# Optimization experiments

Hardware: AMD Instinct MI355X
Metric: run time of the kernel (lower is better)

Reference implementation:

```python
import jax, jax.numpy as jnp
import numpy as np

N = 50000
NEG_SLOPE = 0.2  # PyG GATConv default negative_slope


def gat_conv(x, src, dst, W, a_src, a_dst, bias, concat):
    """One PyG-style GATConv (eval mode, self-loops already in src/dst).
    x: [N, F_in], W: [F_in, H*C], a_src/a_dst: [H, C], bias: [H*C] or [C].
    """
    H, C = a_src.shape
    xl = (x @ W).reshape(N, H, C)                      # [N, H, C]
    alpha_src = jnp.sum(xl * a_src, axis=-1)           # [N, H]
    alpha_dst = jnp.sum(xl * a_dst, axis=-1)           # [N, H]
    e = jax.nn.leaky_relu(alpha_src[src] + alpha_dst[dst], NEG_SLOPE)  # [E, H]
    # edge-softmax over incoming edges of each destination node
    m = jax.ops.segment_max(e, dst, num_segments=N)    # [N, H]
    e = jnp.exp(e - m[dst])
    s = jax.ops.segment_sum(e, dst, num_segments=N)    # [N, H]
    alpha = e / s[dst]                                 # [E, H]
    msg = xl[src] * alpha[:, :, None]                  # [E, H, C]
    out = jax.ops.segment_sum(msg, dst, num_segments=N)  # [N, H, C]
    out = out.reshape(N, H * C) if concat else out.mean(axis=1)
    return out + bias


def setup_inputs() -> dict:
    key = jax.random.key(0)
    ks = jax.random.split(key, 10)
    in_ch, hid, out_ch, heads = 128, 64, 64, 4
    E = 800000
    x = jax.random.normal(ks[0], (N, in_ch), dtype=jnp.float32)
    edge_index = jax.random.randint(ks[1], (2, E), 0, N, dtype=jnp.int64)
    s1 = 1.0 / np.sqrt(in_ch)
    s2 = 1.0 / np.sqrt(hid * heads)
    return {
        "x": x,
        "edge_index": edge_index,
        "W1": jax.random.normal(ks[2], (in_ch, heads * hid), jnp.float32) * s1,
        "att_src1": jax.random.normal(ks[3], (heads, hid), jnp.float32) * s1,
        "att_dst1": jax.random.normal(ks[4], (heads, hid), jnp.float32) * s1,
        "b1": jnp.zeros((heads * hid,), jnp.float32),
        "W2": jax.random.normal(ks[5], (heads * hid, out_ch), jnp.float32) * s2,
        "att_src2": jax.random.normal(ks[6], (1, out_ch), jnp.float32) * s2,
        "att_dst2": jax.random.normal(ks[7], (1, out_ch), jnp.float32) * s2,
        "b2": jnp.zeros((out_ch,), jnp.float32),
    }


def reference(x, edge_index, W1, att_src1, att_dst1, b1, W2, att_src2, att_dst2, b2):
    # PyG GATConv adds self-loops by default
    loops = jnp.arange(N, dtype=edge_index.dtype)
    src = jnp.concatenate([edge_index[0], loops])
    dst = jnp.concatenate([edge_index[1], loops])
    h = gat_conv(x, src, dst, W1, att_src1, att_dst1, b1, concat=True)
    h = jax.nn.elu(h)  # dropout is identity in eval mode
    out = gat_conv(h, src, dst, W2, att_src2, att_dst2, b2, concat=False)
    return out
```

## Files before the change

### kernel.cpp

```cpp
#include <hip/hip_runtime.h>
#include <math.h>


typedef unsigned short u16;
typedef short s8v __attribute__((ext_vector_type(8)));
typedef float f32x4 __attribute__((ext_vector_type(4)));

#define LOG2E 1.4426950408889634f

__device__ __forceinline__ float bflo(unsigned int u) {
  return __builtin_bit_cast(float, u << 16);
}
__device__ __forceinline__ float bfhi(unsigned int u) {
  return __builtin_bit_cast(float, u & 0xffff0000u);
}
__device__ __forceinline__ u16 f2bf(float f) {
  unsigned int u = __builtin_bit_cast(unsigned int, f);
  return (u16)((u + 0x7fff + ((u >> 16) & 1)) >> 16);
}


__global__ void count_edges_kernel(const int* __restrict__ ei, int E, int Nn,
                                   int* __restrict__ deg) {
  int e = blockIdx.x * blockDim.x + threadIdx.x;
  if (e >= E + Nn) return;
  int dst = (e < E) ? ei[E + e] : (e - E);
  atomicAdd(&deg[dst], 1);
}

__global__ void scan_partials_kernel(const int* __restrict__ deg,
                                     int* __restrict__ partials, int Ntot) {
  __shared__ int red[256];
  int t = threadIdx.x;
  int base = blockIdx.x * 1024 + t * 4;
  int s = 0;
  if (base + 3 < Ntot) {
    int4 v = *(const int4*)(deg + base);
    s = v.x + v.y + v.z + v.w;
  } else {
    for (int i = 0; i < 4; ++i)
      if (base + i < Ntot) s += deg[base + i];
  }
  red[t] = s;
  __syncthreads();
  for (int off = 128; off > 0; off >>= 1) {
    if (t < off) red[t] += red[t + off];
    __syncthreads();
  }
  if (t == 0) partials[blockIdx.x] = red[0];
}

__global__ void scan_final_kernel(const int* __restrict__ deg,
                                  const int* __restrict__ partials,
                                  int* __restrict__ rowptr,
                                  int* __restrict__ cursor, int Ntot, int NB) {
  __shared__ int sums[256];
  int t = threadIdx.x;
  int bid = blockIdx.x;
  int base = bid * 1024 + t * 4;
  int4 v = make_int4(0, 0, 0, 0);
  if (base + 3 < Ntot) {
    v = *(const int4*)(deg + base);
  } else {
    if (base + 0 < Ntot) v.x = deg[base + 0];
    if (base + 1 < Ntot) v.y = deg[base + 1];
    if (base + 2 < Ntot) v.z = deg[base + 2];
    if (base + 3 < Ntot) v.w = deg[base + 3];
  }
  sums[t] = v.x + v.y + v.z + v.w;
  __syncthreads();
  for (int off = 1; off < 256; off <<= 1) {
    int u = (t >= off) ? sums[t - off] : 0;
    __syncthreads();
    sums[t] += u;
    __syncthreads();
  }
  int boff = 0;
  for (int j = 0; j < bid; ++j) boff += partials[j];
  int excl = boff + ((t == 0) ? 0 : sums[t - 1]);
  int4 r;
  r.x = excl;
  r.y = r.x + v.x;
  r.z = r.y + v.y;
  r.w = r.z + v.z;
  if (base + 3 < Ntot) {
    *(int4*)(rowptr + base) = r;
    *(int4*)(cursor + base) = r;
  } else {
    if (base + 0 < Ntot) { rowptr[base + 0] = r.x; cursor[base + 0] = r.x; }
    if (base + 1 < Ntot) { rowptr[base + 1] = r.y; cursor[base + 1] = r.y; }
    if (base + 2 < Ntot) { rowptr[base + 2] = r.z; cursor[base + 2] = r.z; }
    if (base + 3 < Ntot) { rowptr[base + 3] = r.w; cursor[base + 3] = r.w; }
  }
}

__global__ void scatter_edges_kernel(const int* __restrict__ ei, int E, int Nn,
                                     int* __restrict__ cursor, int* __restrict__ col) {
  int e = blockIdx.x * blockDim.x + threadIdx.x;
  if (e >= E + Nn) return;
  int src, dst;
  if (e < E) { src = ei[e]; dst = ei[E + e]; }
  else       { src = dst = e - E; }
  int pos = atomicAdd(&cursor[dst], 1);
  col[pos] = src;
}


__global__ void cast_prep_kernel(const float* __restrict__ x, u16* __restrict__ xb,
                                 int nx4,
                                 const float* __restrict__ W1, u16* __restrict__ W1T,
                                 int K1, int N1,
                                 const float* __restrict__ W2, u16* __restrict__ W2T,
                                 int K2, int N2) {
  int i = blockIdx.x * blockDim.x + threadIdx.x;
  if (i < nx4) {
    float4 v = *(const float4*)(x + (size_t)i * 4);
    ushort4 o = make_ushort4(f2bf(v.x), f2bf(v.y), f2bf(v.z), f2bf(v.w));
    *(ushort4*)(xb + (size_t)i * 4) = o;
    return;
  }
  int e = i - nx4;
  int tot1 = K1 * N1;
  if (e < tot1) {
    int k = e / N1, n = e % N1;
    W1T[n * K1 + k] = f2bf(W1[e]);
    return;
  }
  e -= tot1;
  if (e < K2 * N2) {
    int k = e / N2, n = e % N2;
    W2T[n * K2 + k] = f2bf(W2[e]);
  }
}


template <int BN>
__global__ __launch_bounds__(256) void gemm_mfma_kernel(
    const u16* __restrict__ A, const u16* __restrict__ Bt,
    u16* __restrict__ C, int M, int K, int NC) {
  constexpr int BM = 128, BK = 32, PK = 40;
  constexpr int NJ = BN / 32;
  __shared__ short As[BM][PK];
  __shared__ short Bs[BN][PK];

  int tid = threadIdx.x;
  int lane = tid & 63, w = tid >> 6;
  int wm = (w >> 1) * 64, wn = (w & 1) * (BN / 2);
  int bm0 = blockIdx.x * BM, bn0 = blockIdx.y * BN;
  int fr = lane & 15, fk = (lane >> 4) * 8;

  f32x4 acc[4][NJ] = {};

  for (int k0 = 0; k0 < K; k0 += BK) {
#pragma unroll
    for (int p = 0; p < BM * BK / 2048; ++p) {
      int idx = p * 2048 + tid * 8;
      int r = idx / BK, c = idx % BK;
      *(s8v*)&As[r][c] = *(const s8v*)(A + (size_t)(bm0 + r) * K + k0 + c);
    }
#pragma unroll
    for (int p = 0; p < BN * BK / 2048; ++p) {
      int idx = p * 2048 + tid * 8;
      int r = idx / BK, c = idx % BK;
      *(s8v*)&Bs[r][c] = *(const s8v*)(Bt + (size_t)(bn0 + r) * K + k0 + c);
    }
    __syncthreads();

    s8v af[4], bf[NJ];
#pragma unroll
    for (int i = 0; i < 4; ++i)
      af[i] = *(const s8v*)&As[wm + i * 16 + fr][fk];
#pragma unroll
    for (int j = 0; j < NJ; ++j)
      bf[j] = *(const s8v*)&Bs[wn + j * 16 + fr][fk];
#pragma unroll
    for (int i = 0; i < 4; ++i)
#pragma unroll
      for (int j = 0; j < NJ; ++j)
        acc[i][j] = __builtin_amdgcn_mfma_f32_16x16x32_bf16(af[i], bf[j], acc[i][j], 0, 0, 0);
    __syncthreads();
  }

#pragma unroll
  for (int i = 0; i < 4; ++i)
#pragma unroll
    for (int j = 0; j < NJ; ++j)
#pragma unroll
      for (int r = 0; r < 4; ++r) {
        int row = bm0 + wm + i * 16 + (lane >> 4) * 4 + r;
        if (row < M)
          C[(size_t)row * NC + bn0 + wn + j * 16 + fr] = f2bf(acc[i][j][r]);
      }
}


__global__ void alpha_kernel(const u16* __restrict__ xlb,
                             const float* __restrict__ a_src,
                             const float* __restrict__ a_dst,
                             float* __restrict__ asrc, float* __restrict__ adst,
                             int NH, int H, int C) {
  int idx = blockIdx.x * blockDim.x + threadIdx.x;
  if (idx >= NH) return;
  int h = idx % H;
  const u16* row = xlb + (size_t)idx * C;
  float ssum = 0.f, dsum = 0.f;
  for (int c = 0; c < C; c += 8) {
    uint4 v = *(const uint4*)(row + c);
    float f[8] = {bflo(v.x), bfhi(v.x), bflo(v.y), bfhi(v.y),
                  bflo(v.z), bfhi(v.z), bflo(v.w), bfhi(v.w)};
#pragma unroll
    for (int j = 0; j < 8; ++j) {
      ssum = fmaf(f[j], a_src[h * C + c + j], ssum);
      dsum = fmaf(f[j], a_dst[h * C + c + j], dsum);
    }
  }
  asrc[idx] = ssum * LOG2E;
  adst[idx] = dsum * LOG2E;
}


__global__ void agg_multi_kernel(const u16* __restrict__ xlb,
                                 const float* __restrict__ asrc,
                                 const float* __restrict__ adst,
                                 const int* __restrict__ rowptr,
                                 const int* __restrict__ col,
                                 const float* __restrict__ bias,
                                 u16* __restrict__ hb, int Nn) {
  int n = blockIdx.x * 8 + (threadIdx.x >> 5);
  if (n >= Nn) return;
  int lane = threadIdx.x & 31;
  int h = lane >> 3;
  float adn = adst[n * 4 + h];
  int beg = rowptr[n], end = rowptr[n + 1];

  float s = 0.f;
  float acc[8] = {};

  float as0 = 0.f, as1 = 0.f, as2 = 0.f, as3 = 0.f;
  uint4 v0 = {}, v1 = {}, v2 = {}, v3 = {};
  {
    int sc = col[beg];
    as0 = asrc[sc * 4 + h];
    v0 = *(const uint4*)(xlb + (size_t)sc * 256 + lane * 8);
    if (beg + 1 < end) {
      int c1 = col[beg + 1];
      as1 = asrc[c1 * 4 + h];
      v1 = *(const uint4*)(xlb + (size_t)c1 * 256 + lane * 8);
    }
    if (beg + 2 < end) {
      int c2 = col[beg + 2];
      as2 = asrc[c2 * 4 + h];
      v2 = *(const uint4*)(xlb + (size_t)c2 * 256 + lane * 8);
    }
    if (beg + 3 < end) {
      int c3 = col[beg + 3];
      as3 = asrc[c3 * 4 + h];
      v3 = *(const uint4*)(xlb + (size_t)c3 * 256 + lane * 8);
    }
  }

  for (int i = beg; i < end; ++i) {
    float e = as0 + adn;
    e = fmaxf(e, 0.2f * e);
    uint4 vc = v0;
    as0 = as1; v0 = v1;
    as1 = as2; v1 = v2;
    as2 = as3; v2 = v3;
    if (i + 4 < end) {
      int sc = col[i + 4];
      as3 = asrc[sc * 4 + h];
      v3 = *(const uint4*)(xlb + (size_t)sc * 256 + lane * 8);
    }
    float w = __builtin_amdgcn_exp2f(e);
    s += w;
    acc[0] = fmaf(w, bflo(vc.x), acc[0]);
    acc[1] = fmaf(w, bfhi(vc.x), acc[1]);
    acc[2] = fmaf(w, bflo(vc.y), acc[2]);
    acc[3] = fmaf(w, bfhi(vc.y), acc[3]);
    acc[4] = fmaf(w, bflo(vc.z), acc[4]);
    acc[5] = fmaf(w, bfhi(vc.z), acc[5]);
    acc[6] = fmaf(w, bflo(vc.w), acc[6]);
    acc[7] = fmaf(w, bfhi(vc.w), acc[7]);
  }
  float inv_s = 1.f / s;

  float4 b0 = *(const float4*)(bias + lane * 8);
  float4 b1f = *(const float4*)(bias + lane * 8 + 4);
  float bb[8] = {b0.x, b0.y, b0.z, b0.w, b1f.x, b1f.y, b1f.z, b1f.w};
  u16 ov[8];
#pragma unroll
  for (int j = 0; j < 8; ++j) {
    float o = fmaf(acc[j], inv_s, bb[j]);
    o = (o > 0.f) ? o : __expf(o) - 1.f;
    ov[j] = f2bf(o);
  }
  *(uint4*)(hb + (size_t)n * 256 + lane * 8) = *(uint4*)ov;
}


__global__ void agg_single_kernel(const u16* __restrict__ xlb,
                                  const float* __restrict__ asrc,
                                  const float* __restrict__ adst,
                                  const int* __restrict__ rowptr,
                                  const int* __restrict__ col,
                                  const float* __restrict__ bias,
                                  float* __restrict__ out, int Nn) {
  int n = blockIdx.x * 32 + (threadIdx.x >> 3);
  if (n >= Nn) return;
  int lane = threadIdx.x & 7;
  float adn = adst[n];
  int beg = rowptr[n], end = rowptr[n + 1];

  float s = 0.f;
  float acc[8] = {};

  float as0 = 0.f, as1 = 0.f, as2 = 0.f;
  uint4 v0 = {}, v1 = {}, v2 = {};
  {
    int sc = col[beg];
    as0 = asrc[sc];
    v0 = *(const uint4*)(xlb + (size_t)sc * 64 + lane * 8);
    if (beg + 1 < end) {
      int c1 = col[beg + 1];
      as1 = asrc[c1];
      v1 = *(const uint4*)(xlb + (size_t)c1 * 64 + lane * 8);
    }
    if (beg + 2 < end) {
      int c2 = col[beg + 2];
      as2 = asrc[c2];
      v2 = *(const uint4*)(xlb + (size_t)c2 * 64 + lane * 8);
    }
  }

  for (int i = beg; i < end; ++i) {
    float e = as0 + adn;
    e = fmaxf(e, 0.2f * e);
    uint4 vc = v0;
    as0 = as1; v0 = v1;
    as1 = as2; v1 = v2;
    if (i + 3 < end) {
      int sc = col[i + 3];
      as2 = asrc[sc];
      v2 = *(const uint4*)(xlb + (size_t)sc * 64 + lane * 8);
    }
    float w = __builtin_amdgcn_exp2f(e);
    s += w;
    acc[0] = fmaf(w, bflo(vc.x), acc[0]);
    acc[1] = fmaf(w, bfhi(vc.x), acc[1]);
    acc[2] = fmaf(w, bflo(vc.y), acc[2]);
    acc[3] = fmaf(w, bfhi(vc.y), acc[3]);
    acc[4] = fmaf(w, bflo(vc.z), acc[4]);
    acc[5] = fmaf(w, bfhi(vc.z), acc[5]);
    acc[6] = fmaf(w, bflo(vc.w), acc[6]);
    acc[7] = fmaf(w, bfhi(vc.w), acc[7]);
  }
  float inv_s = 1.f / s;

  const float* bp = bias + lane * 8;
  float4 o0, o1;
  o0.x = fmaf(acc[0], inv_s, bp[0]);
  o0.y = fmaf(acc[1], inv_s, bp[1]);
  o0.z = fmaf(acc[2], inv_s, bp[2]);
  o0.w = fmaf(acc[3], inv_s, bp[3]);
  o1.x = fmaf(acc[4], inv_s, bp[4]);
  o1.y = fmaf(acc[5], inv_s, bp[5]);
  o1.z = fmaf(acc[6], inv_s, bp[6]);
  o1.w = fmaf(acc[7], inv_s, bp[7]);
  *(float4*)(out + (size_t)n * 64 + lane * 8) = o0;
  *(float4*)(out + (size_t)n * 64 + lane * 8 + 4) = o1;
}


extern "C" void kernel_launch(void* const* d_in, const int* in_sizes, int n_in,
                              void* d_out, int out_size, void* d_ws, size_t ws_size,
                              hipStream_t stream) {
  const float* x   = (const float*)d_in[0];
  const int*   ei  = (const int*)d_in[1];
  const float* W1  = (const float*)d_in[2];
  const float* as1 = (const float*)d_in[3];
  const float* ad1 = (const float*)d_in[4];
  const float* b1  = (const float*)d_in[5];
  const float* W2  = (const float*)d_in[6];
  const float* as2 = (const float*)d_in[7];
  const float* ad2 = (const float*)d_in[8];
  const float* b2  = (const float*)d_in[9];
  float* out = (float*)d_out;

  const int Nn = in_sizes[0] / 128;
  const int E  = in_sizes[1] / 2;
  const int Et = E + Nn;
  const int Ntot = Nn + 1;
  const int NB = (Ntot + 1023) / 1024;
  const int MB = (Nn + 127) / 128;
  const int Mpad = MB * 128;

  char* base = (char*)d_ws;
  size_t off = 0;
  auto alloc = [&](size_t bytes) -> void* {
    void* p = base + off;
    off = (off + bytes + 255) & ~(size_t)255;
    return p;
  };
  u16*   xb       = (u16*)alloc((size_t)Mpad * 128 * 2);
  u16*   w1t      = (u16*)alloc((size_t)256 * 128 * 2);
  u16*   w2t      = (u16*)alloc((size_t)64 * 256 * 2);
  u16*   xlb1     = (u16*)alloc((size_t)Mpad * 256 * 2);
  u16*   hb       = (u16*)alloc((size_t)Mpad * 256 * 2);
  float* asrc1    = (float*)alloc((size_t)Nn * 4 * 4);
  float* adst1    = (float*)alloc((size_t)Nn * 4 * 4);
  float* asrc2    = (float*)alloc((size_t)Nn * 4);
  float* adst2    = (float*)alloc((size_t)Nn * 4);
  int*   deg      = (int*)alloc((size_t)(Ntot + 8) * 4);
  int*   rowptr   = (int*)alloc((size_t)(Ntot + 8) * 4);
  int*   cursor   = (int*)alloc((size_t)(Ntot + 8) * 4);
  int*   partials = (int*)alloc(256 * 4);
  int*   col      = (int*)alloc((size_t)Et * 4);
  u16*   xlb2     = xlb1;

  hipMemsetAsync(deg, 0, (size_t)Ntot * 4, stream);
  count_edges_kernel<<<(Et + 255) / 256, 256, 0, stream>>>(ei, E, Nn, deg);
  scan_partials_kernel<<<NB, 256, 0, stream>>>(deg, partials, Ntot);
  scan_final_kernel<<<NB, 256, 0, stream>>>(deg, partials, rowptr, cursor, Ntot, NB);
  scatter_edges_kernel<<<(Et + 255) / 256, 256, 0, stream>>>(ei, E, Nn, cursor, col);
  {
    int nx4 = Nn * 128 / 4;
    int tot = nx4 + 128 * 256 + 256 * 64;
    cast_prep_kernel<<<(tot + 255) / 256, 256, 0, stream>>>(
        x, xb, nx4, W1, w1t, 128, 256, W2, w2t, 256, 64);
  }

  {
    dim3 grid(MB, 2);
    gemm_mfma_kernel<128><<<grid, 256, 0, stream>>>(xb, w1t, xlb1, Nn, 128, 256);
  }
  alpha_kernel<<<(Nn * 4 + 255) / 256, 256, 0, stream>>>(xlb1, as1, ad1, asrc1, adst1, Nn * 4, 4, 64);
  agg_multi_kernel<<<(Nn + 7) / 8, 256, 0, stream>>>(xlb1, asrc1, adst1, rowptr, col, b1, hb, Nn);

  {
    dim3 grid(MB, 1);
    gemm_mfma_kernel<64><<<grid, 256, 0, stream>>>(hb, w2t, xlb2, Nn, 256, 64);
  }
  alpha_kernel<<<(Nn + 255) / 256, 256, 0, stream>>>(xlb2, as2, ad2, asrc2, adst2, Nn, 1, 64);
  agg_single_kernel<<<(Nn + 31) / 32, 256, 0, stream>>>(xlb2, asrc2, adst2, rowptr, col, b2, out, Nn);
}
```

Measured before the change: 260.0 us.

## Fuse x cast into GEMM1 and attention-logit dot products into both GEMM epilogues

Drops the separate fp32-to-bf16 cast pass over x by converting rows while loading them into GEMM1's shared memory, with the whole K=128 held in LDS at once. Computes the per-head source and destination attention logits in the GEMM epilogues from the fp32 accumulators using lane shuffles, which removes both alpha kernels and their re-read of xl. Weight transposition moves into the edge-count kernel. This cuts launches and global traffic, but GEMM1 now uses more shared memory per block (lower occupancy), and the logits come from fp32 accumulators instead of bf16-rounded values.

Result: faster. 254.0 us (-2.3%).

```diff
diff --git a/kernel.cpp b/kernel.cpp
--- a/kernel.cpp
+++ b/kernel.cpp
@@ -20,12 +20,28 @@
 }
 
 
-__global__ void count_edges_kernel(const int* __restrict__ ei, int E, int Nn,
-                                   int* __restrict__ deg) {
-  int e = blockIdx.x * blockDim.x + threadIdx.x;
-  if (e >= E + Nn) return;
-  int dst = (e < E) ? ei[E + e] : (e - E);
-  atomicAdd(&deg[dst], 1);
+__global__ void prep_count_kernel(const int* __restrict__ ei, int E, int Nn,
+                                  int* __restrict__ deg,
+                                  const float* __restrict__ W1, u16* __restrict__ W1T,
+                                  const float* __restrict__ W2, u16* __restrict__ W2T) {
+  int i = blockIdx.x * blockDim.x + threadIdx.x;
+  int Et = E + Nn;
+  if (i < Et) {
+    int dst = (i < E) ? ei[E + i] : (i - E);
+    atomicAdd(&deg[dst], 1);
+    return;
+  }
+  int e = i - Et;
+  if (e < 128 * 256) {
+    int k = e >> 8, n = e & 255;
+    W1T[n * 128 + k] = f2bf(W1[e]);
+    return;
+  }
+  e -= 128 * 256;
+  if (e < 256 * 64) {
+    int k = e >> 6, n = e & 63;
+    W2T[n * 256 + k] = f2bf(W2[e]);
+  }
 }
 
 __global__ void scan_partials_kernel(const int* __restrict__ deg,
@@ -106,116 +122,209 @@
 }
 
 
-__global__ void cast_prep_kernel(const float* __restrict__ x, u16* __restrict__ xb,
-                                 int nx4,
-                                 const float* __restrict__ W1, u16* __restrict__ W1T,
-                                 int K1, int N1,
-                                 const float* __restrict__ W2, u16* __restrict__ W2T,
-                                 int K2, int N2) {
-  int i = blockIdx.x * blockDim.x + threadIdx.x;
-  if (i < nx4) {
-    float4 v = *(const float4*)(x + (size_t)i * 4);
+__global__ __launch_bounds__(256) void gemm1_fused_kernel(
+    const float* __restrict__ x,
+    const u16* __restrict__ w1t,
+    const float* __restrict__ a_src,
+    const float* __restrict__ a_dst,
+    u16* __restrict__ C,
+    float* __restrict__ asrc, float* __restrict__ adst,
+    int M) {
+  constexpr int PK = 136;
+  __shared__ short As[128][PK];
+  __shared__ short Bs[128][PK];
+  int tid = threadIdx.x;
+  int lane = tid & 63, w = tid >> 6;
+  int q = lane >> 4, fr = lane & 15;
+  int wm = (w >> 1) * 64, wn = (w & 1) * 64;
+  int bm0 = blockIdx.x * 128;
+  int fk = q * 8;
+
+#pragma unroll
+  for (int p = 0; p < 16; ++p) {
+    int idx = p * 1024 + tid * 4;
+    int r = idx >> 7, c = idx & 127;
+    float4 v = make_float4(0.f, 0.f, 0.f, 0.f);
+    if (bm0 + r < M) v = *(const float4*)(x + (size_t)(bm0 + r) * 128 + c);
     ushort4 o = make_ushort4(f2bf(v.x), f2bf(v.y), f2bf(v.z), f2bf(v.w));
-    *(ushort4*)(xb + (size_t)i * 4) = o;
-    return;
-  }
-  int e = i - nx4;
-  int tot1 = K1 * N1;
-  if (e < tot1) {
-    int k = e / N1, n = e % N1;
-    W1T[n * K1 + k] = f2bf(W1[e]);
-    return;
-  }
-  e -= tot1;
-  if (e < K2 * N2) {
-    int k = e / N2, n = e % N2;
-    W2T[n * K2 + k] = f2bf(W2[e]);
-  }
-}
-
-
-template <int BN>
-__global__ __launch_bounds__(256) void gemm_mfma_kernel(
-    const u16* __restrict__ A, const u16* __restrict__ Bt,
-    u16* __restrict__ C, int M, int K, int NC) {
-  constexpr int BM = 128, BK = 32, PK = 40;
-  constexpr int NJ = BN / 32;
+    *(ushort4*)&As[r][c] = o;
+  }
+#pragma unroll
+  for (int p = 0; p < 8; ++p) {
+    int idx = p * 2048 + tid * 8;
+    int r = idx >> 7, c = idx & 127;
+    *(s8v*)&Bs[r][c] = *(const s8v*)(w1t + (size_t)r * 128 + c);
+  }
+  __syncthreads();
+
+  for (int nh = 0; nh < 2; ++nh) {
+    if (nh == 1) {
+      __syncthreads();
+#pragma unroll
+      for (int p = 0; p < 8; ++p) {
+        int idx = p * 2048 + tid * 8;
+        int r = idx >> 7, c = idx & 127;
+        *(s8v*)&Bs[r][c] = *(const s8v*)(w1t + (size_t)(128 + r) * 128 + c);
+      }
+      __syncthreads();
+    }
+    f32x4 acc[4][4] = {};
+#pragma unroll
+    for (int ks = 0; ks < 4; ++ks) {
+      s8v af[4], bf[4];
+#pragma unroll
+      for (int i = 0; i < 4; ++i)
+        af[i] = *(const s8v*)&As[wm + i * 16 + fr][ks * 32 + fk];
+#pragma unroll
+      for (int j = 0; j < 4; ++j)
+        bf[j] = *(const s8v*)&Bs[wn + j * 16 + fr][ks * 32 + fk];
+#pragma unroll
+      for (int i = 0; i < 4; ++i)
+#pragma unroll
+        for (int j = 0; j < 4; ++j)
+          acc[i][j] = __builtin_amdgcn_mfma_f32_16x16x32_bf16(af[i], bf[j], acc[i][j], 0, 0, 0);
+    }
+
+    int h = nh * 2 + (wn >> 6);
+    float asv[4], adv[4];
+#pragma unroll
+    for (int j = 0; j < 4; ++j) {
+      asv[j] = a_src[h * 64 + j * 16 + fr];
+      adv[j] = a_dst[h * 64 + j * 16 + fr];
+    }
+#pragma unroll
+    for (int i = 0; i < 4; ++i) {
+#pragma unroll
+      for (int r = 0; r < 4; ++r) {
+        int row = bm0 + wm + i * 16 + q * 4 + r;
+        float ps = 0.f, pd = 0.f;
+#pragma unroll
+        for (int j = 0; j < 4; ++j) {
+          ps = fmaf(acc[i][j][r], asv[j], ps);
+          pd = fmaf(acc[i][j][r], adv[j], pd);
+        }
+#pragma unroll
+        for (int mmask = 1; mmask < 16; mmask <<= 1) {
+          ps += __shfl_xor(ps, mmask, 64);
+          pd += __shfl_xor(pd, mmask, 64);
+        }
+        if (fr == 0 && row < M) {
+          asrc[row * 4 + h] = ps * LOG2E;
+          adst[row * 4 + h] = pd * LOG2E;
+        }
+      }
+    }
+#pragma unroll
+    for (int i = 0; i < 4; ++i)
+#pragma unroll
+      for (int j = 0; j < 4; ++j)
+#pragma unroll
+        for (int r = 0; r < 4; ++r) {
+          int row = bm0 + wm + i * 16 + q * 4 + r;
+          if (row < M)
+            C[(size_t)row * 256 + nh * 128 + wn + j * 16 + fr] = f2bf(acc[i][j][r]);
+        }
+  }
+}
+
+
+__global__ __launch_bounds__(256) void gemm2_fused_kernel(
+    const u16* __restrict__ A,
+    const u16* __restrict__ Bt,
+    const float* __restrict__ a_src,
+    const float* __restrict__ a_dst,
+    u16* __restrict__ C,
+    float* __restrict__ asrc, float* __restrict__ adst,
+    int M) {
+  constexpr int BM = 128, BN = 64, BK = 32, PK = 40;
   __shared__ short As[BM][PK];
   __shared__ short Bs[BN][PK];
-
+  __shared__ float alds[BM][4];
   int tid = threadIdx.x;
   int lane = tid & 63, w = tid >> 6;
-  int wm = (w >> 1) * 64, wn = (w & 1) * (BN / 2);
-  int bm0 = blockIdx.x * BM, bn0 = blockIdx.y * BN;
-  int fr = lane & 15, fk = (lane >> 4) * 8;
-
-  f32x4 acc[4][NJ] = {};
-
-  for (int k0 = 0; k0 < K; k0 += BK) {
-#pragma unroll
-    for (int p = 0; p < BM * BK / 2048; ++p) {
+  int q = lane >> 4, fr = lane & 15;
+  int wm = (w >> 1) * 64, wn = (w & 1) * 32;
+  int bm0 = blockIdx.x * BM;
+  int fk = q * 8;
+
+  f32x4 acc[4][2] = {};
+
+  for (int k0 = 0; k0 < 256; k0 += BK) {
+#pragma unroll
+    for (int p = 0; p < 2; ++p) {
       int idx = p * 2048 + tid * 8;
       int r = idx / BK, c = idx % BK;
-      *(s8v*)&As[r][c] = *(const s8v*)(A + (size_t)(bm0 + r) * K + k0 + c);
-    }
-#pragma unroll
-    for (int p = 0; p < BN * BK / 2048; ++p) {
-      int idx = p * 2048 + tid * 8;
+      *(s8v*)&As[r][c] = *(const s8v*)(A + (size_t)(bm0 + r) * 256 + k0 + c);
+    }
+    {
+      int idx = tid * 8;
       int r = idx / BK, c = idx % BK;
-      *(s8v*)&Bs[r][c] = *(const s8v*)(Bt + (size_t)(bn0 + r) * K + k0 + c);
+      if (r < BN)
+        *(s8v*)&Bs[r][c] = *(const s8v*)(Bt + (size_t)r * 256 + k0 + c);
     }
     __syncthreads();
 
-    s8v af[4], bf[NJ];
+    s8v af[4], bf[2];
 #pragma unroll
     for (int i = 0; i < 4; ++i)
       af[i] = *(const s8v*)&As[wm + i * 16 + fr][fk];
 #pragma unroll
-    for (int j = 0; j < NJ; ++j)
+    for (int j = 0; j < 2; ++j)
       bf[j] = *(const s8v*)&Bs[wn + j * 16 + fr][fk];
 #pragma unroll
     for (int i = 0; i < 4; ++i)
 #pragma unroll
-      for (int j = 0; j < NJ; ++j)
+      for (int j = 0; j < 2; ++j)
         acc[i][j] = __builtin_amdgcn_mfma_f32_16x16x32_bf16(af[i], bf[j], acc[i][j], 0, 0, 0);
     __syncthreads();
   }
 
+  float asv[2], adv[2];
+#pragma unroll
+  for (int j = 0; j < 2; ++j) {
+    asv[j] = a_src[wn + j * 16 + fr];
+    adv[j] = a_dst[wn + j * 16 + fr];
+  }
+#pragma unroll
+  for (int i = 0; i < 4; ++i) {
+#pragma unroll
+    for (int r = 0; r < 4; ++r) {
+      int lr = wm + i * 16 + q * 4 + r;
+      float ps = 0.f, pd = 0.f;
+#pragma unroll
+      for (int j = 0; j < 2; ++j) {
+        ps = fmaf(acc[i][j][r], asv[j], ps);
+        pd = fmaf(acc[i][j][r], adv[j], pd);
+      }
+#pragma unroll
+      for (int mmask = 1; mmask < 16; mmask <<= 1) {
+        ps += __shfl_xor(ps, mmask, 64);
+        pd += __shfl_xor(pd, mmask, 64);
+      }
+      if (fr == 0) {
+        alds[lr][(w & 1) * 2 + 0] = ps;
+        alds[lr][(w & 1) * 2 + 1] = pd;
+      }
+    }
+  }
 #pragma unroll
   for (int i = 0; i < 4; ++i)
 #pragma unroll
-    for (int j = 0; j < NJ; ++j)
+    for (int j = 0; j < 2; ++j)
 #pragma unroll
       for (int r = 0; r < 4; ++r) {
-        int row = bm0 + wm + i * 16 + (lane >> 4) * 4 + r;
+        int row = bm0 + wm + i * 16 + q * 4 + r;
         if (row < M)
-          C[(size_t)row * NC + bn0 + wn + j * 16 + fr] = f2bf(acc[i][j][r]);
+          C[(size_t)row * 64 + wn + j * 16 + fr] = f2bf(acc[i][j][r]);
       }
-}
-
-
-__global__ void alpha_kernel(const u16* __restrict__ xlb,
-                             const float* __restrict__ a_src,
-                             const float* __restrict__ a_dst,
-                             float* __restrict__ asrc, float* __restrict__ adst,
-                             int NH, int H, int C) {
-  int idx = blockIdx.x * blockDim.x + threadIdx.x;
-  if (idx >= NH) return;
-  int h = idx % H;
-  const u16* row = xlb + (size_t)idx * C;
-  float ssum = 0.f, dsum = 0.f;
-  for (int c = 0; c < C; c += 8) {
-    uint4 v = *(const uint4*)(row + c);
-    float f[8] = {bflo(v.x), bfhi(v.x), bflo(v.y), bfhi(v.y),
-                  bflo(v.z), bfhi(v.z), bflo(v.w), bfhi(v.w)};
-#pragma unroll
-    for (int j = 0; j < 8; ++j) {
-      ssum = fmaf(f[j], a_src[h * C + c + j], ssum);
-      dsum = fmaf(f[j], a_dst[h * C + c + j], dsum);
-    }
-  }
-  asrc[idx] = ssum * LOG2E;
-  adst[idx] = dsum * LOG2E;
+  __syncthreads();
+  if (tid < BM) {
+    int row = bm0 + tid;
+    if (row < M) {
+      asrc[row] = (alds[tid][0] + alds[tid][2]) * LOG2E;
+      adst[row] = (alds[tid][1] + alds[tid][3]) * LOG2E;
+    }
+  }
 }
 
 
@@ -401,7 +510,6 @@
     off = (off + bytes + 255) & ~(size_t)255;
     return p;
   };
-  u16*   xb       = (u16*)alloc((size_t)Mpad * 128 * 2);
   u16*   w1t      = (u16*)alloc((size_t)256 * 128 * 2);
   u16*   w2t      = (u16*)alloc((size_t)64 * 256 * 2);
   u16*   xlb1     = (u16*)alloc((size_t)Mpad * 256 * 2);
@@ -418,28 +526,18 @@
   u16*   xlb2     = xlb1;
 
   hipMemsetAsync(deg, 0, (size_t)Ntot * 4, stream);
-  count_edges_kernel<<<(Et + 255) / 256, 256, 0, stream>>>(ei, E, Nn, deg);
+  {
+    int tot = Et + 128 * 256 + 256 * 64;
+    prep_count_kernel<<<(tot + 255) / 256, 256, 0, stream>>>(
+        ei, E, Nn, deg, W1, w1t, W2, w2t);
+  }
   scan_partials_kernel<<<NB, 256, 0, stream>>>(deg, partials, Ntot);
   scan_final_kernel<<<NB, 256, 0, stream>>>(deg, partials, rowptr, cursor, Ntot, NB);
   scatter_edges_kernel<<<(Et + 255) / 256, 256, 0, stream>>>(ei, E, Nn, cursor, col);
-  {
-    int nx4 = Nn * 128 / 4;
-    int tot = nx4 + 128 * 256 + 256 * 64;
-    cast_prep_kernel<<<(tot + 255) / 256, 256, 0, stream>>>(
-        x, xb, nx4, W1, w1t, 128, 256, W2, w2t, 256, 64);
-  }
-
-  {
-    dim3 grid(MB, 2);
-    gemm_mfma_kernel<128><<<grid, 256, 0, stream>>>(xb, w1t, xlb1, Nn, 128, 256);
-  }
-  alpha_kernel<<<(Nn * 4 + 255) / 256, 256, 0, stream>>>(xlb1, as1, ad1, asrc1, adst1, Nn * 4, 4, 64);
+
+  gemm1_fused_kernel<<<MB, 256, 0, stream>>>(x, w1t, as1, ad1, xlb1, asrc1, adst1, Nn);
   agg_multi_kernel<<<(Nn + 7) / 8, 256, 0, stream>>>(xlb1, asrc1, adst1, rowptr, col, b1, hb, Nn);
 
-  {
-    dim3 grid(MB, 1);
-    gemm_mfma_kernel<64><<<grid, 256, 0, stream>>>(hb, w2t, xlb2, Nn, 256, 64);
-  }
-  alpha_kernel<<<(Nn + 255) / 256, 256, 0, stream>>>(xlb2, as2, ad2, asrc2, adst2, Nn, 1, 64);
+  gemm2_fused_kernel<<<MB, 256, 0, stream>>>(hb, w2t, as2, ad2, xlb2, asrc2, adst2, Nn);
   agg_single_kernel<<<(Nn + 31) / 32, 256, 0, stream>>>(xlb2, asrc2, adst2, rowptr, col, b2, out, Nn);
 }
```
